# Performance work log

Measured on AMD Instinct MI355X. Metric: run time of the kernel, lower is better.

The kernel has to match this reference:

```python
import jax, jax.numpy as jnp
import numpy as np

ROOT_2 = 1.41421
C = 256
DIV = 4
CP = C // DIV  # 64


def _spectral_normalize(w2d):
    # exact largest singular value (torch uses power iteration approx of this)
    s = jnp.linalg.norm(w2d, ord=2)
    return w2d / s


def setup_inputs() -> dict:
    key = jax.random.key(0)
    ks = jax.random.split(key, 10)
    B, H, W = 8, 64, 64
    x = jax.random.normal(ks[0], (B, C, H, W), dtype=jnp.float32)
    # 1x1 conv weights stored as [out, in]; spectral-normalized like torch's spectral_norm
    def conv_w(k, o, i):
        w = jax.random.normal(k, (o, i), dtype=jnp.float32) * (1.0 / np.sqrt(i))
        return _spectral_normalize(w)
    Wq = conv_w(ks[1], CP, C); bq = jnp.zeros((CP,), jnp.float32)
    Wk = conv_w(ks[2], CP, C); bk = jnp.zeros((CP,), jnp.float32)
    Wv = conv_w(ks[3], CP, C); bv = jnp.zeros((CP,), jnp.float32)
    Wo = conv_w(ks[4], C, CP); bo = jnp.zeros((C,), jnp.float32)
    gamma = jnp.zeros((1,), jnp.float32)
    return {"x": x, "Wq": Wq, "bq": bq, "Wk": Wk, "bk": bk,
            "Wv": Wv, "bv": bv, "Wo": Wo, "bo": bo, "gamma": gamma}


def reference(x, Wq, bq, Wk, bk, Wv, bv, Wo, bo, gamma):
    B, c, h, w = x.shape
    n = h * w
    const1 = jnp.float32(ROOT_2 / np.sqrt(C))       # Weight_Scaling(in_channels)
    const2 = jnp.float32(ROOT_2 / np.sqrt(CP))      # Weight_Scaling(in_channels//div_num)
    xs = (const1 * x).reshape(B, c, n)              # [B,C,N]
    q = jnp.einsum('oc,bcn->bon', Wq, xs) + bq[None, :, None]  # [B,C',N]
    k = jnp.einsum('oc,bcn->bon', Wk, xs) + bk[None, :, None]
    v = jnp.einsum('oc,bcn->bon', Wv, xs) + bv[None, :, None]
    # attn[b,i,j] = softmax_j(q[:,i]^T k[:,j])
    scores = jnp.einsum('bcn,bcm->bnm', q, k)       # [B,N,N]
    attn = jax.nn.softmax(scores, axis=-1)
    sa = jnp.einsum('bcm,bnm->bcn', v, attn)        # v @ attn^T
    sa = const2 * sa
    out = jnp.einsum('oc,bcn->bon', Wo, sa) + bo[None, :, None]  # [B,C,N]
    out = out.reshape(B, c, h, w)
    return gamma[0] * out + x
```

## Files before the change

kernel.cpp:

```cpp
#include <hip/hip_runtime.h>


#define Bsz 8
#define Cch 256
#define CPd 64
#define Nn  4096
#define TIL 64
#define NSPL 2
#define MHALF (Nn / NSPL)

typedef __attribute__((ext_vector_type(8))) short short8;
typedef __attribute__((ext_vector_type(4))) float f32x4;

static constexpr float C1 = (float)(1.41421 / 16.0);
static constexpr float C2 = (float)(1.41421 / 8.0);

__device__ inline unsigned pk_trunc(float lo, float hi) {
    return __builtin_amdgcn_perm(__float_as_uint(hi), __float_as_uint(lo), 0x07060302u);
}

__global__ __launch_bounds__(256) void wconv_kernel(
    const float* __restrict__ Wq, const float* __restrict__ Wk,
    const float* __restrict__ Wv, const float* __restrict__ Wo,
    unsigned short* __restrict__ Wb)
{
    const int idx = (blockIdx.x * 256 + threadIdx.x) * 4;
    const float* src = (idx < 16384) ? Wq : (idx < 32768) ? Wk : (idx < 49152) ? Wv : Wo;
    const float4 v = *(const float4*)(src + (idx & 16383));
    *(uint2*)(Wb + idx) = make_uint2(pk_trunc(v.x, v.y), pk_trunc(v.z, v.w));
}

__global__ __launch_bounds__(256) void qkv_kernel(
    const float* __restrict__ x, const unsigned short* __restrict__ Wb,
    const float* __restrict__ bq, const float* __restrict__ bk, const float* __restrict__ bv,
    unsigned short* __restrict__ qT, unsigned short* __restrict__ kT,
    unsigned short* __restrict__ vB)
{
    __shared__ __align__(16) float T[TIL * 68];

    const int b   = blockIdx.y;
    const int n0  = blockIdx.x * TIL;
    const int t   = threadIdx.x;
    const int g   = t >> 6;
    const int l15 = t & 15;
    const int l4  = (t & 63) >> 4;

    const float* xb = x + (size_t)b * Cch * Nn + n0 + 16 * g + l15;
    short8 xf[8];
    #pragma unroll
    for (int ks = 0; ks < 8; ++ks) {
        float xr[8];
        #pragma unroll
        for (int j = 0; j < 8; ++j)
            xr[j] = C1 * xb[(size_t)(8 * l4 + 32 * ks + j) * Nn];
        union { unsigned u[4]; short8 s; } p;
        p.u[0] = pk_trunc(xr[0], xr[1]); p.u[1] = pk_trunc(xr[2], xr[3]);
        p.u[2] = pk_trunc(xr[4], xr[5]); p.u[3] = pk_trunc(xr[6], xr[7]);
        xf[ks] = p.s;
    }

    #pragma unroll
    for (int mat = 0; mat < 3; ++mat) {
        const unsigned short* W = Wb + mat * 16384;
        const float* bias = (mat == 0) ? bq : (mat == 1) ? bk : bv;

        f32x4 acc[4];
        #pragma unroll
        for (int st = 0; st < 4; ++st) {
            const float bb = bias[16 * st + l15];
            acc[st] = (f32x4){bb, bb, bb, bb};
        }
        #pragma unroll
        for (int st = 0; st < 4; ++st) {
            #pragma unroll
            for (int ks = 0; ks < 8; ++ks) {
                const short8 wf = *(const short8*)&W[(16 * st + l15) * Cch + 8 * l4 + 32 * ks];
                acc[st] = __builtin_amdgcn_mfma_f32_16x16x32_bf16(xf[ks], wf, acc[st], 0, 0, 0);
            }
        }

        __syncthreads();
        if (mat < 2) {
            #pragma unroll
            for (int st = 0; st < 4; ++st)
                #pragma unroll
                for (int r = 0; r < 4; ++r)
                    T[(16 * g + 4 * l4 + r) * 68 + 16 * st + l15] = acc[st][r];
        } else {
            #pragma unroll
            for (int st = 0; st < 4; ++st)
                #pragma unroll
                for (int r = 0; r < 4; ++r)
                    T[(16 * st + l15) * 68 + 16 * g + 4 * l4 + r] = acc[st][r];
        }
        __syncthreads();

        const int row = t >> 2;
        const int sg  = 16 * (t & 3);
        const float4 a0 = *(const float4*)&T[row * 68 + sg + 0];
        const float4 a1 = *(const float4*)&T[row * 68 + sg + 4];
        const float4 a2 = *(const float4*)&T[row * 68 + sg + 8];
        const float4 a3 = *(const float4*)&T[row * 68 + sg + 12];
        const uint4 lo = make_uint4(pk_trunc(a0.x, a0.y), pk_trunc(a0.z, a0.w),
                                    pk_trunc(a1.x, a1.y), pk_trunc(a1.z, a1.w));
        const uint4 hi = make_uint4(pk_trunc(a2.x, a2.y), pk_trunc(a2.z, a2.w),
                                    pk_trunc(a3.x, a3.y), pk_trunc(a3.z, a3.w));
        unsigned short* dst;
        if (mat < 2) {
            dst = (mat == 0 ? qT : kT) + ((size_t)(b * Nn + n0 + row)) * CPd + sg;
        } else {
            dst = vB + ((size_t)(b * CPd + row)) * Nn + n0 + sg;
        }
        *(uint4*)dst = lo;
        *(uint4*)(dst + 8) = hi;
    }
}

__global__ __launch_bounds__(256, 4) void flash_kernel(
    const unsigned short* __restrict__ qT, const unsigned short* __restrict__ kT,
    const unsigned short* __restrict__ vB, float* __restrict__ Op, float* __restrict__ Lg)
{
    __shared__ __align__(16) unsigned short Ks[TIL * 72];
    __shared__ __align__(16) unsigned short Vs[TIL * 72];
    __shared__ __align__(16) float Ps[TIL * 68];
    __shared__ float Lsh[TIL];

    const int b   = blockIdx.y;
    const int n0  = blockIdx.x * TIL;
    const int s   = blockIdx.z;
    const int t   = threadIdx.x;
    const int l   = t & 63;
    const int g   = t >> 6;
    const int l15 = l & 15;
    const int l4  = l >> 4;

    if (t < TIL) Lsh[t] = 0.f;

    const unsigned short* qp = qT + (size_t)(b * Nn + n0 + 16 * g + l15) * CPd + 8 * l4;
    const short8 qf0 = *(const short8*)qp;
    const short8 qf1 = *(const short8*)(qp + 32);

    f32x4 acco[4];
    #pragma unroll
    for (int ct = 0; ct < 4; ++ct) acco[ct] = (f32x4){0.f, 0.f, 0.f, 0.f};
    float Lp[4] = {0.f, 0.f, 0.f, 0.f};

    const uint4* kg = (const uint4*)(kT + (size_t)b * Nn * CPd);
    const unsigned short* vb = vB + (size_t)b * CPd * Nn;
    const int mbase = s * MHALF;

    for (int mi = 0; mi < MHALF; mi += TIL) {
        const int m0 = mbase + mi;
        __syncthreads();
        {
            const int r = t >> 3, cc = t & 7;
            uint4 k0 = kg[(m0 + r) * 8 + cc];
            uint4 k1 = kg[(m0 + r + 32) * 8 + cc];
            *(uint4*)&Ks[r * 72 + 8 * cc]        = k0;
            *(uint4*)&Ks[(r + 32) * 72 + 8 * cc] = k1;
            uint4 w0 = *(const uint4*)(vb + (size_t)r * Nn + m0 + 8 * cc);
            uint4 w1 = *(const uint4*)(vb + (size_t)(r + 32) * Nn + m0 + 8 * cc);
            *(uint4*)&Vs[r * 72 + 8 * cc]        = w0;
            *(uint4*)&Vs[(r + 32) * 72 + 8 * cc] = w1;
        }
        __syncthreads();

        f32x4 accs[4];
        #pragma unroll
        for (int st = 0; st < 4; ++st) {
            accs[st] = (f32x4){0.f, 0.f, 0.f, 0.f};
            const short8 kf0 = *(const short8*)&Ks[(16 * st + l15) * 72 + 8 * l4];
            const short8 kf1 = *(const short8*)&Ks[(16 * st + l15) * 72 + 8 * l4 + 32];
            accs[st] = __builtin_amdgcn_mfma_f32_16x16x32_bf16(qf0, kf0, accs[st], 0, 0, 0);
            accs[st] = __builtin_amdgcn_mfma_f32_16x16x32_bf16(qf1, kf1, accs[st], 0, 0, 0);
        }

        #pragma unroll
        for (int st = 0; st < 4; ++st) {
            #pragma unroll
            for (int r = 0; r < 4; ++r) {
                float p = __expf(accs[st][r]);
                Lp[r] += p;
                Ps[(16 * g + 4 * l4 + r) * 68 + 16 * st + l15] = p;
            }
        }
        __syncthreads();

        #pragma unroll
        for (int ks = 0; ks < 2; ++ks) {
            const float4 a0 = *(const float4*)&Ps[(16 * g + l15) * 68 + 8 * l4 + 32 * ks];
            const float4 a1 = *(const float4*)&Ps[(16 * g + l15) * 68 + 8 * l4 + 32 * ks + 4];
            union { unsigned u[4]; short8 s8; } pu;
            pu.u[0] = pk_trunc(a0.x, a0.y); pu.u[1] = pk_trunc(a0.z, a0.w);
            pu.u[2] = pk_trunc(a1.x, a1.y); pu.u[3] = pk_trunc(a1.z, a1.w);
            #pragma unroll
            for (int ct = 0; ct < 4; ++ct) {
                const short8 vf = *(const short8*)&Vs[(16 * ct + l15) * 72 + 8 * l4 + 32 * ks];
                acco[ct] = __builtin_amdgcn_mfma_f32_16x16x32_bf16(pu.s8, vf, acco[ct], 0, 0, 0);
            }
        }
    }

    #pragma unroll
    for (int r = 0; r < 4; ++r) atomicAdd(&Lsh[16 * g + 4 * l4 + r], Lp[r]);
    __syncthreads();

    float* ob = Op + ((size_t)(s * Bsz + b) * Nn + n0) * CPd;
    #pragma unroll
    for (int r = 0; r < 4; ++r) {
        const int nl = 16 * g + 4 * l4 + r;
        #pragma unroll
        for (int ct = 0; ct < 4; ++ct)
            ob[(size_t)nl * CPd + 16 * ct + l15] = acco[ct][r];
    }
    if (t < TIL) Lg[(size_t)(s * Bsz + b) * Nn + n0 + t] = Lsh[t];
}

__global__ __launch_bounds__(256) void out_kernel(
    const float* __restrict__ Op, const float* __restrict__ Lg,
    const unsigned short* __restrict__ Wob,
    const float* __restrict__ bo, const float* __restrict__ gamma,
    const float* __restrict__ x, float* __restrict__ y)
{
    __shared__ __align__(16) unsigned short Wos[Cch * 72];
    __shared__ __align__(16) unsigned short Sas[TIL * 72];
    __shared__ float bos[Cch];

    const int b   = blockIdx.y;
    const int n0  = blockIdx.x * TIL;
    const int t   = threadIdx.x;
    const int l   = t & 63;
    const int g   = t >> 6;
    const int l15 = l & 15;
    const int l4  = l >> 4;

    bos[t] = bo[t];
    {
        const uint4* wg = (const uint4*)Wob;
        #pragma unroll
        for (int p = 0; p < 8; ++p) {
            const int idx = p * 256 + t;
            const int row = idx >> 3, seg = idx & 7;
            *(uint4*)&Wos[row * 72 + seg * 8] = wg[idx];
        }
        const int n = t >> 2, seg = t & 3;
        const float* o0 = Op + ((size_t)(b * Nn + n0 + n)) * CPd + seg * 16;
        const float* o1 = o0 + (size_t)Bsz * Nn * CPd;
        const float l0 = Lg[(size_t)b * Nn + n0 + n];
        const float l1 = Lg[(size_t)(Bsz + b) * Nn + n0 + n];
        const float sc = C2 / (l0 + l1);
        unsigned pk[8];
        #pragma unroll
        for (int i = 0; i < 4; ++i) {
            const float4 a = ((const float4*)o0)[i];
            const float4 c = ((const float4*)o1)[i];
            pk[2 * i]     = pk_trunc((a.x + c.x) * sc, (a.y + c.y) * sc);
            pk[2 * i + 1] = pk_trunc((a.z + c.z) * sc, (a.w + c.w) * sc);
        }
        *(uint4*)&Sas[n * 72 + seg * 16]     = make_uint4(pk[0], pk[1], pk[2], pk[3]);
        *(uint4*)&Sas[n * 72 + seg * 16 + 8] = make_uint4(pk[4], pk[5], pk[6], pk[7]);
    }
    __syncthreads();

    short8 bfr[4][2];
    #pragma unroll
    for (int ns = 0; ns < 4; ++ns) {
        bfr[ns][0] = *(const short8*)&Sas[(16 * ns + l15) * 72 + 8 * l4];
        bfr[ns][1] = *(const short8*)&Sas[(16 * ns + l15) * 72 + 8 * l4 + 32];
    }
    const float gam = gamma[0];
    const float* xb = x + (size_t)b * Cch * Nn;
    float*       yb = y + (size_t)b * Cch * Nn;

    #pragma unroll
    for (int os = 0; os < 4; ++os) {
        const int obase = 64 * g + 16 * os;
        const short8 af0 = *(const short8*)&Wos[(obase + l15) * 72 + 8 * l4];
        const short8 af1 = *(const short8*)&Wos[(obase + l15) * 72 + 8 * l4 + 32];
        #pragma unroll
        for (int ns = 0; ns < 4; ++ns) {
            f32x4 acc = (f32x4){0.f, 0.f, 0.f, 0.f};
            acc = __builtin_amdgcn_mfma_f32_16x16x32_bf16(af0, bfr[ns][0], acc, 0, 0, 0);
            acc = __builtin_amdgcn_mfma_f32_16x16x32_bf16(af1, bfr[ns][1], acc, 0, 0, 0);
            #pragma unroll
            for (int r = 0; r < 4; ++r) {
                const int o = obase + 4 * l4 + r;
                const size_t idx = (size_t)o * Nn + n0 + 16 * ns + l15;
                yb[idx] = fmaf(gam, acc[r] + bos[o], xb[idx]);
            }
        }
    }
}

extern "C" void kernel_launch(void* const* d_in, const int* in_sizes, int n_in,
                              void* d_out, int out_size, void* d_ws, size_t ws_size,
                              hipStream_t stream)
{
    (void)in_sizes; (void)n_in; (void)out_size; (void)ws_size;
    const float* x     = (const float*)d_in[0];
    const float* Wq    = (const float*)d_in[1];
    const float* bq    = (const float*)d_in[2];
    const float* Wk    = (const float*)d_in[3];
    const float* bk    = (const float*)d_in[4];
    const float* Wv    = (const float*)d_in[5];
    const float* bv    = (const float*)d_in[6];
    const float* Wo    = (const float*)d_in[7];
    const float* bo    = (const float*)d_in[8];
    const float* gamma = (const float*)d_in[9];
    float* y = (float*)d_out;

    const size_t per = (size_t)Bsz * Nn * CPd;
    unsigned short* qT = (unsigned short*)d_ws;
    unsigned short* kT = qT + per;
    unsigned short* vB = kT + per;
    float* Op = (float*)(vB + per);
    float* Lg = Op + NSPL * per;
    unsigned short* Wb = (unsigned short*)(Lg + NSPL * Bsz * Nn);

    dim3 grid(Nn / TIL, Bsz);
    dim3 gridF(Nn / TIL, Bsz, NSPL);
    wconv_kernel<<<64, 256, 0, stream>>>(Wq, Wk, Wv, Wo, Wb);
    qkv_kernel<<<grid, 256, 0, stream>>>(x, Wb, bq, bk, bv, qT, kT, vB);
    flash_kernel<<<gridF, 256, 0, stream>>>(qT, kT, vB, Op, Lg);
    out_kernel<<<grid, 256, 0, stream>>>(Op, Lg, Wb + 3 * 16384, bo, gamma, x, y);
}
```

Baseline: 211.6 us.

## Stage QKV weights in LDS, pack softmax probs to bf16 via DPP, widen out kernel

The QKV projection kernel now copies each 64x256 bf16 weight matrix into padded shared memory before the MFMA loop instead of reading fragments from global memory, at the cost of an extra barrier per matrix. The flash kernel pairs neighbouring lanes with a DPP swap to pack P into bf16 before writing it to LDS, which halves the P staging buffer and removes the float reload and conversion. The output kernel moves to 512 threads per block so each wave handles fewer output rows.

```diff
diff --git a/kernel.cpp b/kernel.cpp
--- a/kernel.cpp
+++ b/kernel.cpp
@@ -18,6 +18,10 @@
 __device__ inline unsigned pk_trunc(float lo, float hi) {
     return __builtin_amdgcn_perm(__float_as_uint(hi), __float_as_uint(lo), 0x07060302u);
 }
+__device__ inline float dpp_swap1(float v) {
+    return __uint_as_float((unsigned)__builtin_amdgcn_mov_dpp(
+        (int)__float_as_uint(v), 0xB1, 0xF, 0xF, true));
+}
 
 __global__ __launch_bounds__(256) void wconv_kernel(
     const float* __restrict__ Wq, const float* __restrict__ Wk,
@@ -36,6 +40,7 @@
     unsigned short* __restrict__ qT, unsigned short* __restrict__ kT,
     unsigned short* __restrict__ vB)
 {
+    __shared__ __align__(16) unsigned short Wlds[CPd * 264];
     __shared__ __align__(16) float T[TIL * 68];
 
     const int b   = blockIdx.y;
@@ -61,9 +66,18 @@
 
     #pragma unroll
     for (int mat = 0; mat < 3; ++mat) {
-        const unsigned short* W = Wb + mat * 16384;
+        {
+            const uint4* wg = (const uint4*)(Wb + mat * 16384);
+            #pragma unroll
+            for (int p = 0; p < 8; ++p) {
+                const int idx = p * 256 + t;
+                const int o = idx >> 5, cs = idx & 31;
+                *(uint4*)&Wlds[o * 264 + cs * 8] = wg[idx];
+            }
+        }
+        __syncthreads();
+
         const float* bias = (mat == 0) ? bq : (mat == 1) ? bk : bv;
-
         f32x4 acc[4];
         #pragma unroll
         for (int st = 0; st < 4; ++st) {
@@ -74,12 +88,12 @@
         for (int st = 0; st < 4; ++st) {
             #pragma unroll
             for (int ks = 0; ks < 8; ++ks) {
-                const short8 wf = *(const short8*)&W[(16 * st + l15) * Cch + 8 * l4 + 32 * ks];
+                const short8 wf = *(const short8*)&Wlds[(16 * st + l15) * 264 + 8 * l4 + 32 * ks];
                 acc[st] = __builtin_amdgcn_mfma_f32_16x16x32_bf16(xf[ks], wf, acc[st], 0, 0, 0);
             }
         }
-
-        __syncthreads();
+        __syncthreads();
+
         if (mat < 2) {
             #pragma unroll
             for (int st = 0; st < 4; ++st)
@@ -122,7 +136,7 @@
 {
     __shared__ __align__(16) unsigned short Ks[TIL * 72];
     __shared__ __align__(16) unsigned short Vs[TIL * 72];
-    __shared__ __align__(16) float Ps[TIL * 68];
+    __shared__ __align__(16) unsigned Pb[TIL * 36];
     __shared__ float Lsh[TIL];
 
     const int b   = blockIdx.y;
@@ -133,6 +147,9 @@
     const int g   = t >> 6;
     const int l15 = l & 15;
     const int l4  = l >> 4;
+    const int par = l & 1;
+    const unsigned sel = par ? 0x03020706u : 0x07060302u;
+    const int l15h = l15 >> 1;
 
     if (t < TIL) Lsh[t] = 0.f;
 
@@ -177,26 +194,27 @@
 
         #pragma unroll
         for (int st = 0; st < 4; ++st) {
+            unsigned u[4];
             #pragma unroll
             for (int r = 0; r < 4; ++r) {
                 float p = __expf(accs[st][r]);
                 Lp[r] += p;
-                Ps[(16 * g + 4 * l4 + r) * 68 + 16 * st + l15] = p;
-            }
+                float nb = dpp_swap1(p);
+                u[r] = __builtin_amdgcn_perm(__float_as_uint(nb), __float_as_uint(p), sel);
+            }
+            const int rb = 16 * g + 4 * l4 + 2 * par;
+            Pb[(rb + 0) * 36 + 8 * st + l15h] = u[2 * par];
+            Pb[(rb + 1) * 36 + 8 * st + l15h] = u[2 * par + 1];
         }
         __syncthreads();
 
         #pragma unroll
         for (int ks = 0; ks < 2; ++ks) {
-            const float4 a0 = *(const float4*)&Ps[(16 * g + l15) * 68 + 8 * l4 + 32 * ks];
-            const float4 a1 = *(const float4*)&Ps[(16 * g + l15) * 68 + 8 * l4 + 32 * ks + 4];
-            union { unsigned u[4]; short8 s8; } pu;
-            pu.u[0] = pk_trunc(a0.x, a0.y); pu.u[1] = pk_trunc(a0.z, a0.w);
-            pu.u[2] = pk_trunc(a1.x, a1.y); pu.u[3] = pk_trunc(a1.z, a1.w);
+            const short8 pf = *(const short8*)&Pb[(16 * g + l15) * 36 + 4 * l4 + 16 * ks];
             #pragma unroll
             for (int ct = 0; ct < 4; ++ct) {
                 const short8 vf = *(const short8*)&Vs[(16 * ct + l15) * 72 + 8 * l4 + 32 * ks];
-                acco[ct] = __builtin_amdgcn_mfma_f32_16x16x32_bf16(pu.s8, vf, acco[ct], 0, 0, 0);
+                acco[ct] = __builtin_amdgcn_mfma_f32_16x16x32_bf16(pf, vf, acco[ct], 0, 0, 0);
             }
         }
     }
@@ -216,7 +234,7 @@
     if (t < TIL) Lg[(size_t)(s * Bsz + b) * Nn + n0 + t] = Lsh[t];
 }
 
-__global__ __launch_bounds__(256) void out_kernel(
+__global__ __launch_bounds__(512) void out_kernel(
     const float* __restrict__ Op, const float* __restrict__ Lg,
     const unsigned short* __restrict__ Wob,
     const float* __restrict__ bo, const float* __restrict__ gamma,
@@ -230,19 +248,21 @@
     const int n0  = blockIdx.x * TIL;
     const int t   = threadIdx.x;
     const int l   = t & 63;
-    const int g   = t >> 6;
+    const int w   = t >> 6;
     const int l15 = l & 15;
     const int l4  = l >> 4;
 
-    bos[t] = bo[t];
+    if (t < Cch) bos[t] = bo[t];
     {
         const uint4* wg = (const uint4*)Wob;
         #pragma unroll
-        for (int p = 0; p < 8; ++p) {
-            const int idx = p * 256 + t;
+        for (int p = 0; p < 4; ++p) {
+            const int idx = p * 512 + t;
             const int row = idx >> 3, seg = idx & 7;
             *(uint4*)&Wos[row * 72 + seg * 8] = wg[idx];
         }
+    }
+    if (t < 256) {
         const int n = t >> 2, seg = t & 3;
         const float* o0 = Op + ((size_t)(b * Nn + n0 + n)) * CPd + seg * 16;
         const float* o1 = o0 + (size_t)Bsz * Nn * CPd;
@@ -273,8 +293,8 @@
     float*       yb = y + (size_t)b * Cch * Nn;
 
     #pragma unroll
-    for (int os = 0; os < 4; ++os) {
-        const int obase = 64 * g + 16 * os;
+    for (int os2 = 0; os2 < 2; ++os2) {
+        const int obase = 16 * (w + 8 * os2);
         const short8 af0 = *(const short8*)&Wos[(obase + l15) * 72 + 8 * l4];
         const short8 af1 = *(const short8*)&Wos[(obase + l15) * 72 + 8 * l4 + 32];
         #pragma unroll
@@ -322,5 +342,5 @@
     wconv_kernel<<<64, 256, 0, stream>>>(Wq, Wk, Wv, Wo, Wb);
     qkv_kernel<<<grid, 256, 0, stream>>>(x, Wb, bq, bk, bv, qT, kT, vB);
     flash_kernel<<<gridF, 256, 0, stream>>>(qT, kT, vB, Op, Lg);
-    out_kernel<<<grid, 256, 0, stream>>>(Op, Lg, Wb + 3 * 16384, bo, gamma, x, y);
-}
+    out_kernel<<<grid, 512, 0, stream>>>(Op, Lg, Wb + 3 * 16384, bo, gamma, x, y);
+}
```

Measured after the change: 187.6 us. 1.13x faster.
